# Kernel tuning notes

Measured on AMD Instinct MI355X. Metric: run time of the kernel, lower is better.

Reference implementation:

```python
import jax, jax.numpy as jnp
import numpy as np

B, S, D, H = 2, 2048, 1024, 16
HD = D // H
SCALE = HD ** -0.5


def _xavier(key, fan_out, fan_in):
    limit = (6.0 / (fan_in + fan_out)) ** 0.5
    return jax.random.uniform(key, (fan_out, fan_in), jnp.float32, -limit, limit)


def setup_inputs() -> dict:
    key = jax.random.key(0)
    ks = jax.random.split(key, 11)
    return {
        "q": jax.random.normal(ks[0], (B, S, D), jnp.float32),
        "k": jax.random.normal(ks[1], (B, S, D), jnp.float32),
        "v": jax.random.normal(ks[2], (B, S, D), jnp.float32),
        "Wq": _xavier(ks[3], D, D), "bq": jnp.zeros((D,), jnp.float32),
        "Wk": _xavier(ks[4], D, D), "bk": jnp.zeros((D,), jnp.float32),
        "Wv": _xavier(ks[5], D, D), "bv": jnp.zeros((D,), jnp.float32),
        "Wo": _xavier(ks[6], D, D), "bo": jnp.zeros((D,), jnp.float32),
    }


def reference(q, k, v, Wq, bq, Wk, bk, Wv, bv, Wo, bo):
    # projections: torch Linear is x @ W.T + b
    def split_heads(x):  # [B,S,D] -> [B,H,S,HD]
        return x.reshape(B, S, H, HD).transpose(0, 2, 1, 3)

    qh = split_heads(q @ Wq.T + bq)
    kh = split_heads(k @ Wk.T + bk)
    vh = split_heads(v @ Wv.T + bv)

    scores = jnp.einsum('bhqd,bhkd->bhqk', qh, kh) * SCALE  # [B,H,S,S]
    attn = jax.nn.softmax(scores, axis=-1)
    out = jnp.einsum('bhqk,bhkd->bhqd', attn, vh)  # [B,H,S,HD]
    out = out.transpose(0, 2, 1, 3).reshape(B, S, D)
    return out @ Wo.T + bo
```

## Files before the change

### kernel.cpp

```cpp
#include <hip/hip_runtime.h>
#include <hip/hip_bf16.h>

typedef __attribute__((ext_vector_type(8))) short bf16x8;
typedef __attribute__((ext_vector_type(4))) float f32x4;
typedef __attribute__((ext_vector_type(16))) float f32x16;
typedef unsigned short u16;

#define MFMA16(A,B,C) __builtin_amdgcn_mfma_f32_16x16x32_bf16(A,B,C,0,0,0)
#define MFMA32(A,B,C) __builtin_amdgcn_mfma_f32_32x32x16_bf16(A,B,C,0,0,0)

__device__ __forceinline__ u16 f2bf(float f) {
    union { float f; unsigned u; } x{f};
    unsigned r = x.u + 0x7FFFu + ((x.u >> 16) & 1u);
    return (u16)(r >> 16);
}

__device__ __forceinline__ unsigned cvtpk(float lo, float hi) {
    unsigned r;
    asm("v_cvt_pk_bf16_f32 %0, %1, %2" : "=v"(r) : "v"(lo), "v"(hi));
    return r;
}

__device__ __forceinline__ void gload16(const void* src, void* dst) {
    __builtin_amdgcn_global_load_lds((const __attribute__((address_space(1))) void*)src,
                                     (__attribute__((address_space(3))) void*)dst, 16, 0, 0);
}

__device__ __forceinline__ void xhalf(unsigned lo, unsigned hi2, int hf, unsigned& j0, unsigned& j2) {
#if __has_builtin(__builtin_amdgcn_permlane32_swap)
    auto r = __builtin_amdgcn_permlane32_swap(lo, hi2, false, false);
    j0 = r[0]; j2 = r[1];
#else
    unsigned olo = (unsigned)__shfl_xor((int)lo, 32);
    unsigned ohi = (unsigned)__shfl_xor((int)hi2, 32);
    j0 = hf ? ohi : lo;
    j2 = hf ? hi2 : olo;
#endif
}

__global__ __launch_bounds__(256)
void cvt_in(const float* __restrict__ a, const float* __restrict__ b, const float* __restrict__ c,
            u16* __restrict__ oa, u16* __restrict__ ob, u16* __restrict__ oc) {
    int blk = blockIdx.x; int which = blk >> 11; int lb = blk & 2047;
    const float* s = which == 0 ? a : (which == 1 ? b : c);
    u16* o = which == 0 ? oa : (which == 1 ? ob : oc);
    size_t base = ((size_t)lb * 256 + threadIdx.x) * 8;
    float4 v0 = *(const float4*)(s + base);
    float4 v1 = *(const float4*)(s + base + 4);
    bf16x8 rv;
    rv[0] = (short)f2bf(v0.x); rv[1] = (short)f2bf(v0.y); rv[2] = (short)f2bf(v0.z); rv[3] = (short)f2bf(v0.w);
    rv[4] = (short)f2bf(v1.x); rv[5] = (short)f2bf(v1.y); rv[6] = (short)f2bf(v1.z); rv[7] = (short)f2bf(v1.w);
    *(bf16x8*)(o + base) = rv;
}

__global__ __launch_bounds__(256)
void cvt_w(const float* __restrict__ a, const float* __restrict__ b, const float* __restrict__ c,
           const float* __restrict__ d, u16* __restrict__ o) {
    int blk = blockIdx.x; int which = blk >> 9; int lb = blk & 511;
    const float* s = which == 0 ? a : (which == 1 ? b : (which == 2 ? c : d));
    size_t base = ((size_t)lb * 256 + threadIdx.x) * 8;
    float4 v0 = *(const float4*)(s + base);
    float4 v1 = *(const float4*)(s + base + 4);
    bf16x8 rv;
    rv[0] = (short)f2bf(v0.x); rv[1] = (short)f2bf(v0.y); rv[2] = (short)f2bf(v0.z); rv[3] = (short)f2bf(v0.w);
    rv[4] = (short)f2bf(v1.x); rv[5] = (short)f2bf(v1.y); rv[6] = (short)f2bf(v1.z); rv[7] = (short)f2bf(v1.w);
    *(bf16x8*)(o + (size_t)which * 1048576 + base) = rv;
}

template<int MODE>
__device__ __forceinline__ void gemm_body(u16* gsm, const u16* __restrict__ A, const u16* __restrict__ W,
                                          const float* __restrict__ bias, void* __restrict__ Cout,
                                          float scale) {
    u16* Asl = gsm;
    u16* Wsl = gsm + 16384;
    const int t = threadIdx.x;
    const int lane = t & 63, w = t >> 6;
    const int g = lane >> 4, c = lane & 15;
    const int bm = blockIdx.y * 128, bn = blockIdx.x * 64;
    const int wr = (w >> 1) * 64, wc = (w & 1) * 32;

    f32x4 acc[4][2];
    #pragma unroll
    for (int i = 0; i < 4; ++i) {
        acc[i][0] = f32x4{0.f, 0.f, 0.f, 0.f};
        acc[i][1] = f32x4{0.f, 0.f, 0.f, 0.f};
    }

#define GS(buf, k0)                                                                         \
    {                                                                                       \
        _Pragma("unroll")                                                                   \
        for (int i = 0; i < 4; ++i) {                                                       \
            int off = i * 4096 + w * 1024 + lane * 16;                                      \
            int row = off >> 7, sl = (off >> 4) & 7;                                        \
            gload16(A + (size_t)(bm + row) * 1024 + (k0) + ((sl ^ (row & 7)) << 3),         \
                    Asl + (buf) * 8192 + i * 2048 + w * 512);                               \
        }                                                                                   \
        _Pragma("unroll")                                                                   \
        for (int i = 0; i < 2; ++i) {                                                       \
            int off = i * 4096 + w * 1024 + lane * 16;                                      \
            int row = off >> 7, sl = (off >> 4) & 7;                                        \
            gload16(W + (size_t)(bn + row) * 1024 + (k0) + ((sl ^ (row & 7)) << 3),         \
                    Wsl + (buf) * 4096 + i * 2048 + w * 512);                               \
        }                                                                                   \
    }

    GS(0, 0);
    __syncthreads();
    int cur = 0;

    for (int k0 = 0; k0 < 1024; k0 += 64) {
        if (k0 < 960) GS(cur ^ 1, k0 + 64);
        #pragma unroll
        for (int ks = 0; ks < 2; ++ks) {
            bf16x8 af[4], bfr[2];
            #pragma unroll
            for (int rf = 0; rf < 4; ++rf) {
                int row = wr + rf * 16 + c;
                int col = (ks * 64 + g * 16) ^ ((row & 7) << 4);
                af[rf] = *(const bf16x8*)((const char*)Asl + cur * 16384 + row * 128 + col);
            }
            #pragma unroll
            for (int cf = 0; cf < 2; ++cf) {
                int row = wc + cf * 16 + c;
                int col = (ks * 64 + g * 16) ^ ((row & 7) << 4);
                bfr[cf] = *(const bf16x8*)((const char*)Wsl + cur * 8192 + row * 128 + col);
            }
            #pragma unroll
            for (int rf = 0; rf < 4; ++rf)
                #pragma unroll
                for (int cf = 0; cf < 2; ++cf)
                    acc[rf][cf] = MFMA16(af[rf], bfr[cf], acc[rf][cf]);
        }
        __syncthreads();
        cur ^= 1;
    }
#undef GS

    if (MODE == 2) {
        u16* trp = gsm;
        #pragma unroll
        for (int rf = 0; rf < 4; ++rf)
            #pragma unroll
            for (int cf = 0; cf < 2; ++cf) {
                int d = wc + cf * 16 + c;
                float bv = bias[bn + d];
                unsigned p0 = cvtpk(acc[rf][cf][0] + bv, acc[rf][cf][1] + bv);
                unsigned p1 = cvtpk(acc[rf][cf][2] + bv, acc[rf][cf][3] + bv);
                *(uint2*)&trp[d * 136 + wr + rf * 16 + 4 * g] = make_uint2(p0, p1);
            }
        __syncthreads();
        const int hb = bn >> 6, bb = bm >> 11, sb = bm & 2047;
        u16* vt = (u16*)Cout;
        #pragma unroll
        for (int i = 0; i < 4; ++i) {
            int fl = t + 256 * i;
            int d = fl >> 4, ch = fl & 15;
            bf16x8 vv = *(const bf16x8*)&trp[d * 136 + ch * 8];
            *(bf16x8*)(vt + ((size_t)((bb * 16 + hb) * 64 + d)) * 2048 + sb + ch * 8) = vv;
        }
        return;
    }

    #pragma unroll
    for (int rf = 0; rf < 4; ++rf) {
        #pragma unroll
        for (int cf = 0; cf < 2; ++cf) {
            int nCol = bn + wc + cf * 16 + c;
            float bv = bias[nCol];
            #pragma unroll
            for (int r = 0; r < 4; ++r) {
                int row = bm + wr + rf * 16 + 4 * g + r;
                float val = (acc[rf][cf][r] + bv) * scale;
                if (MODE == 1) ((float*)Cout)[(size_t)row * 1024 + nCol] = val;
                else           ((u16*)Cout)[(size_t)row * 1024 + nCol] = f2bf(val);
            }
        }
    }
}

__global__ __launch_bounds__(256)
void gemm_qkv(const u16* __restrict__ Ab, const u16* __restrict__ Wb,
              const float* __restrict__ b0, const float* __restrict__ b1, const float* __restrict__ b2,
              u16* __restrict__ Qp, u16* __restrict__ Kp, u16* __restrict__ Vtb, float qscale) {
    __shared__ u16 gsm[24576];
    int z = blockIdx.z;
    if (z == 0)      gemm_body<0>(gsm, Ab,           Wb,           b0, Qp,  qscale);
    else if (z == 1) gemm_body<0>(gsm, Ab + 4194304, Wb + 1048576, b1, Kp,  1.f);
    else             gemm_body<2>(gsm, Ab + 8388608, Wb + 2097152, b2, Vtb, 1.f);
}

__global__ __launch_bounds__(256)
void gemm_o(const u16* __restrict__ A, const u16* __restrict__ W,
            const float* __restrict__ bias, float* __restrict__ out) {
    __shared__ u16 gsm[24576];
    gemm_body<1>(gsm, A, W, bias, out, 1.f);
}

__global__ __launch_bounds__(256)
void attn_mfma(const u16* __restrict__ Qp, const u16* __restrict__ Kp,
               const u16* __restrict__ Vt, u16* __restrict__ AO) {
    __shared__ u16 smem[16384];

    const int t = threadIdx.x, lane = t & 63, w = t >> 6;
    const int c5 = lane & 31, hf = lane >> 5;

    const int id = blockIdx.x;
    const int xcd = id & 7, slot = id >> 3;
    const int hd = xcd * 4 + (slot >> 4);
    const int b = hd >> 4, h = hd & 15;
    const int qw = (slot & 15) * 128 + w * 32;

    bf16x8 qfr[4];
    #pragma unroll
    for (int ks = 0; ks < 4; ++ks)
        qfr[ks] = *(const bf16x8*)(Qp + (size_t)(b * 2048 + qw + c5) * 1024 + h * 64 + ks * 16 + hf * 8);

    f32x16 oacc[2], lacc;
    #pragma unroll
    for (int j = 0; j < 16; ++j) { oacc[0][j] = 0.f; oacc[1][j] = 0.f; lacc[j] = 0.f; }

    bf16x8 ones;
    #pragma unroll
    for (int j = 0; j < 8; ++j) ones[j] = (short)0x3F80;

#define STAGE(buf, kt)                                                                              \
    {                                                                                               \
        _Pragma("unroll")                                                                           \
        for (int i = 0; i < 2; ++i) {                                                               \
            int fl = t + 256 * i;                                                                   \
            int row = fl >> 3, sl = fl & 7;                                                         \
            const u16* srck = Kp + (size_t)(b * 2048 + (kt) * 64 + row) * 1024 + h * 64 +           \
                              ((sl ^ (row & 7)) << 3);                                              \
            gload16(srck, smem + (buf) * 4096 + i * 2048 + w * 512);                                \
            const u16* srcv = Vt + ((size_t)((b * 16 + h) * 64 + row)) * 2048 + (kt) * 64 +         \
                              ((sl ^ (row & 7)) << 3);                                              \
            gload16(srcv, smem + 8192 + (buf) * 4096 + i * 2048 + w * 512);                         \
        }                                                                                           \
    }

    STAGE(0, 0);
    __syncthreads();
    int cur = 0;

    for (int kt = 0; kt < 32; ++kt) {
        if (kt < 31) STAGE(cur ^ 1, kt + 1);
        const char* kbase = (const char*)smem + cur * 8192;
        const char* vbase = (const char*)smem + 16384 + cur * 8192;

        #pragma unroll
        for (int kf = 0; kf < 2; ++kf) {
            f32x16 s;
            #pragma unroll
            for (int j = 0; j < 16; ++j) s[j] = 0.f;
            const int krow = kf * 32 + c5;
            const int ksw = (krow & 7) << 4;
            __builtin_amdgcn_s_setprio(1);
            #pragma unroll
            for (int ks = 0; ks < 4; ++ks) {
                bf16x8 ka = *(const bf16x8*)(kbase + krow * 128 + ((ks * 32 + hf * 16) ^ ksw));
                s = MFMA32(ka, qfr[ks], s);
            }
            __builtin_amdgcn_s_setprio(0);

            #pragma unroll
            for (int j = 0; j < 16; ++j) s[j] = exp2f(s[j]);
            unsigned wd[8];
            #pragma unroll
            for (int j = 0; j < 8; ++j) wd[j] = cvtpk(s[2 * j], s[2 * j + 1]);

            union { unsigned u[4]; bf16x8 v; } p0, p1;
            xhalf(wd[0], wd[2], hf, p0.u[0], p0.u[2]);
            xhalf(wd[1], wd[3], hf, p0.u[1], p0.u[3]);
            xhalf(wd[4], wd[6], hf, p1.u[0], p1.u[2]);
            xhalf(wd[5], wd[7], hf, p1.u[1], p1.u[3]);

            __builtin_amdgcn_s_setprio(1);
            #pragma unroll
            for (int pp = 0; pp < 2; ++pp) {
                bf16x8 pB = pp ? p1.v : p0.v;
                const int kc = kf * 64 + pp * 32 + hf * 16;
                #pragma unroll
                for (int df = 0; df < 2; ++df) {
                    int vrow = df * 32 + c5;
                    bf16x8 va = *(const bf16x8*)(vbase + vrow * 128 + (kc ^ ((vrow & 7) << 4)));
                    oacc[df] = MFMA32(va, pB, oacc[df]);
                }
                lacc = MFMA32(ones, pB, lacc);
            }
            __builtin_amdgcn_s_setprio(0);
        }

        __syncthreads();
        cur ^= 1;
    }

    const float inv = 1.f / lacc[0];
    char* pw = (char*)smem + w * 4096;
    #pragma unroll
    for (int df = 0; df < 2; ++df)
        #pragma unroll
        for (int rq = 0; rq < 4; ++rq) {
            unsigned p0 = cvtpk(oacc[df][rq * 4 + 0] * inv, oacc[df][rq * 4 + 1] * inv);
            unsigned p1 = cvtpk(oacc[df][rq * 4 + 2] * inv, oacc[df][rq * 4 + 3] * inv);
            int dbyte = df * 64 + rq * 16 + hf * 8;
            *(uint2*)(pw + c5 * 128 + (dbyte ^ ((c5 & 7) << 4))) = make_uint2(p0, p1);
        }
    #pragma unroll
    for (int i = 0; i < 4; ++i) {
        int fl = lane + 64 * i;
        int q = fl >> 3, ch = fl & 7;
        bf16x8 vv = *(const bf16x8*)(pw + q * 128 + ((ch * 16) ^ ((q & 7) << 4)));
        *(bf16x8*)(AO + (size_t)(b * 2048 + qw + q) * 1024 + h * 64 + ch * 8) = vv;
    }
}

extern "C" void kernel_launch(void* const* d_in, const int* in_sizes, int n_in,
                              void* d_out, int out_size, void* d_ws, size_t ws_size,
                              hipStream_t stream) {
    const float* q  = (const float*)d_in[0];
    const float* k  = (const float*)d_in[1];
    const float* v  = (const float*)d_in[2];
    const float* Wq = (const float*)d_in[3];
    const float* bq = (const float*)d_in[4];
    const float* Wk = (const float*)d_in[5];
    const float* bk = (const float*)d_in[6];
    const float* Wv = (const float*)d_in[7];
    const float* bv = (const float*)d_in[8];
    const float* Wo = (const float*)d_in[9];
    const float* bo = (const float*)d_in[10];

    const size_t NE = 4194304;
    u16* ws = (u16*)d_ws;
    u16* xq = ws;
    u16* xk = ws + NE;
    u16* xv = ws + 2 * NE;
    u16* Wb = ws + 3 * NE;
    u16* Qp = ws + 4 * NE;
    u16* Kp = ws + 5 * NE;
    u16* Vtb = ws + 6 * NE;
    u16* AO = xk;

    const float CS = 0.125f * 1.4426950408889634f;

    cvt_in<<<6144, 256, 0, stream>>>(q, k, v, xq, xk, xv);
    cvt_w<<<2048, 256, 0, stream>>>(Wq, Wk, Wv, Wo, Wb);

    gemm_qkv<<<dim3(16, 32, 3), 256, 0, stream>>>(ws, Wb, bq, bk, bv, Qp, Kp, Vtb, CS);

    attn_mfma<<<512, 256, 0, stream>>>(Qp, Kp, Vtb, AO);

    gemm_o<<<dim3(16, 32), 256, 0, stream>>>(AO, Wb + 3145728, bo, (float*)d_out);
}
```

Measured before the change: 129.4 us.

## Enlarge GEMM tiles to 128x128 and split attention KV range across two wave groups

The projection GEMMs move from 128x64 to 128x128 block tiles with 4x4 MFMA fragments per wave. In exchange they drop double buffering for a single-buffered load-then-sync loop with setprio around the MFMAs. The V-transpose epilogue is rewritten to go through LDS in two passes. The attention kernel now uses 512 threads, where two groups of four waves each process half of the KV tiles, and the partial outputs and row sums are combined through LDS at the end. This aims to raise wave count per block and per-block GEMM reuse, at the cost of exposed load latency and extra reduction and synchronisation.

```diff
diff --git a/kernel.cpp b/kernel.cpp
--- a/kernel.cpp
+++ b/kernel.cpp
@@ -72,91 +72,85 @@
                                           const float* __restrict__ bias, void* __restrict__ Cout,
                                           float scale) {
     u16* Asl = gsm;
-    u16* Wsl = gsm + 16384;
+    u16* Wsl = gsm + 8192;
     const int t = threadIdx.x;
     const int lane = t & 63, w = t >> 6;
     const int g = lane >> 4, c = lane & 15;
-    const int bm = blockIdx.y * 128, bn = blockIdx.x * 64;
-    const int wr = (w >> 1) * 64, wc = (w & 1) * 32;
-
-    f32x4 acc[4][2];
-    #pragma unroll
-    for (int i = 0; i < 4; ++i) {
-        acc[i][0] = f32x4{0.f, 0.f, 0.f, 0.f};
-        acc[i][1] = f32x4{0.f, 0.f, 0.f, 0.f};
-    }
-
-#define GS(buf, k0)                                                                         \
-    {                                                                                       \
-        _Pragma("unroll")                                                                   \
-        for (int i = 0; i < 4; ++i) {                                                       \
-            int off = i * 4096 + w * 1024 + lane * 16;                                      \
-            int row = off >> 7, sl = (off >> 4) & 7;                                        \
-            gload16(A + (size_t)(bm + row) * 1024 + (k0) + ((sl ^ (row & 7)) << 3),         \
-                    Asl + (buf) * 8192 + i * 2048 + w * 512);                               \
-        }                                                                                   \
-        _Pragma("unroll")                                                                   \
-        for (int i = 0; i < 2; ++i) {                                                       \
-            int off = i * 4096 + w * 1024 + lane * 16;                                      \
-            int row = off >> 7, sl = (off >> 4) & 7;                                        \
-            gload16(W + (size_t)(bn + row) * 1024 + (k0) + ((sl ^ (row & 7)) << 3),         \
-                    Wsl + (buf) * 4096 + i * 2048 + w * 512);                               \
-        }                                                                                   \
-    }
-
-    GS(0, 0);
-    __syncthreads();
-    int cur = 0;
+    const int bm = blockIdx.y * 128, bn = blockIdx.x * 128;
+    const int wr = (w >> 1) * 64, wc = (w & 1) * 64;
+
+    f32x4 acc[4][4];
+    #pragma unroll
+    for (int i = 0; i < 4; ++i)
+        #pragma unroll
+        for (int j = 0; j < 4; ++j) acc[i][j] = f32x4{0.f, 0.f, 0.f, 0.f};
 
     for (int k0 = 0; k0 < 1024; k0 += 64) {
-        if (k0 < 960) GS(cur ^ 1, k0 + 64);
+        __syncthreads();
+        #pragma unroll
+        for (int i = 0; i < 4; ++i) {
+            int off = i * 4096 + w * 1024 + lane * 16;
+            int row = off >> 7, sl = (off >> 4) & 7;
+            gload16(A + (size_t)(bm + row) * 1024 + k0 + ((sl ^ (row & 7)) << 3),
+                    Asl + i * 2048 + w * 512);
+            gload16(W + (size_t)(bn + row) * 1024 + k0 + ((sl ^ (row & 7)) << 3),
+                    Wsl + i * 2048 + w * 512);
+        }
+        __syncthreads();
+
         #pragma unroll
         for (int ks = 0; ks < 2; ++ks) {
-            bf16x8 af[4], bfr[2];
+            bf16x8 af[4], bfr[4];
             #pragma unroll
             for (int rf = 0; rf < 4; ++rf) {
                 int row = wr + rf * 16 + c;
                 int col = (ks * 64 + g * 16) ^ ((row & 7) << 4);
-                af[rf] = *(const bf16x8*)((const char*)Asl + cur * 16384 + row * 128 + col);
-            }
-            #pragma unroll
-            for (int cf = 0; cf < 2; ++cf) {
+                af[rf] = *(const bf16x8*)((const char*)Asl + row * 128 + col);
+            }
+            #pragma unroll
+            for (int cf = 0; cf < 4; ++cf) {
                 int row = wc + cf * 16 + c;
                 int col = (ks * 64 + g * 16) ^ ((row & 7) << 4);
-                bfr[cf] = *(const bf16x8*)((const char*)Wsl + cur * 8192 + row * 128 + col);
-            }
+                bfr[cf] = *(const bf16x8*)((const char*)Wsl + row * 128 + col);
+            }
+            __builtin_amdgcn_s_setprio(1);
             #pragma unroll
             for (int rf = 0; rf < 4; ++rf)
                 #pragma unroll
-                for (int cf = 0; cf < 2; ++cf)
+                for (int cf = 0; cf < 4; ++cf)
                     acc[rf][cf] = MFMA16(af[rf], bfr[cf], acc[rf][cf]);
-        }
-        __syncthreads();
-        cur ^= 1;
-    }
-#undef GS
+            __builtin_amdgcn_s_setprio(0);
+        }
+    }
 
     if (MODE == 2) {
-        u16* trp = gsm;
-        #pragma unroll
-        for (int rf = 0; rf < 4; ++rf)
-            #pragma unroll
-            for (int cf = 0; cf < 2; ++cf) {
-                int d = wc + cf * 16 + c;
-                float bv = bias[bn + d];
-                unsigned p0 = cvtpk(acc[rf][cf][0] + bv, acc[rf][cf][1] + bv);
-                unsigned p1 = cvtpk(acc[rf][cf][2] + bv, acc[rf][cf][3] + bv);
-                *(uint2*)&trp[d * 136 + wr + rf * 16 + 4 * g] = make_uint2(p0, p1);
-            }
-        __syncthreads();
-        const int hb = bn >> 6, bb = bm >> 11, sb = bm & 2047;
+        const int bb = bm >> 11, sb = bm & 2047;
         u16* vt = (u16*)Cout;
         #pragma unroll
-        for (int i = 0; i < 4; ++i) {
-            int fl = t + 256 * i;
-            int d = fl >> 4, ch = fl & 15;
-            bf16x8 vv = *(const bf16x8*)&trp[d * 136 + ch * 8];
-            *(bf16x8*)(vt + ((size_t)((bb * 16 + hb) * 64 + d)) * 2048 + sb + ch * 8) = vv;
+        for (int rd = 0; rd < 2; ++rd) {
+            __syncthreads();
+            if ((w & 1) == rd) {
+                #pragma unroll
+                for (int cf = 0; cf < 4; ++cf) {
+                    int dl = cf * 16 + c;
+                    float bv = bias[bn + rd * 64 + dl];
+                    #pragma unroll
+                    for (int rf = 0; rf < 4; ++rf) {
+                        unsigned p0 = cvtpk(acc[rf][cf][0] + bv, acc[rf][cf][1] + bv);
+                        unsigned p1 = cvtpk(acc[rf][cf][2] + bv, acc[rf][cf][3] + bv);
+                        *(uint2*)&gsm[dl * 136 + wr + rf * 16 + 4 * g] = make_uint2(p0, p1);
+                    }
+                }
+            }
+            __syncthreads();
+            const int hrd = (bn >> 6) + rd;
+            #pragma unroll
+            for (int i = 0; i < 4; ++i) {
+                int idx = i * 256 + t;
+                int d = idx >> 4, ch = idx & 15;
+                bf16x8 vv = *(const bf16x8*)&gsm[d * 136 + ch * 8];
+                *(bf16x8*)(vt + ((size_t)((bb * 16 + hrd) * 64 + d)) * 2048 + sb + ch * 8) = vv;
+            }
         }
         return;
     }
@@ -164,7 +158,7 @@
     #pragma unroll
     for (int rf = 0; rf < 4; ++rf) {
         #pragma unroll
-        for (int cf = 0; cf < 2; ++cf) {
+        for (int cf = 0; cf < 4; ++cf) {
             int nCol = bn + wc + cf * 16 + c;
             float bv = bias[nCol];
             #pragma unroll
@@ -182,7 +176,7 @@
 void gemm_qkv(const u16* __restrict__ Ab, const u16* __restrict__ Wb,
               const float* __restrict__ b0, const float* __restrict__ b1, const float* __restrict__ b2,
               u16* __restrict__ Qp, u16* __restrict__ Kp, u16* __restrict__ Vtb, float qscale) {
-    __shared__ u16 gsm[24576];
+    __shared__ u16 gsm[16384];
     int z = blockIdx.z;
     if (z == 0)      gemm_body<0>(gsm, Ab,           Wb,           b0, Qp,  qscale);
     else if (z == 1) gemm_body<0>(gsm, Ab + 4194304, Wb + 1048576, b1, Kp,  1.f);
@@ -192,23 +186,24 @@
 __global__ __launch_bounds__(256)
 void gemm_o(const u16* __restrict__ A, const u16* __restrict__ W,
             const float* __restrict__ bias, float* __restrict__ out) {
-    __shared__ u16 gsm[24576];
+    __shared__ u16 gsm[16384];
     gemm_body<1>(gsm, A, W, bias, out, 1.f);
 }
 
-__global__ __launch_bounds__(256)
+__global__ __launch_bounds__(512, 4)
 void attn_mfma(const u16* __restrict__ Qp, const u16* __restrict__ Kp,
                const u16* __restrict__ Vt, u16* __restrict__ AO) {
-    __shared__ u16 smem[16384];
+    __shared__ u16 smem[32768];
 
     const int t = threadIdx.x, lane = t & 63, w = t >> 6;
+    const int wl = w & 3, half = w >> 2;
     const int c5 = lane & 31, hf = lane >> 5;
 
     const int id = blockIdx.x;
     const int xcd = id & 7, slot = id >> 3;
     const int hd = xcd * 4 + (slot >> 4);
     const int b = hd >> 4, h = hd & 15;
-    const int qw = (slot & 15) * 128 + w * 32;
+    const int qw = (slot & 15) * 128 + wl * 32;
 
     bf16x8 qfr[4];
     #pragma unroll
@@ -223,18 +218,18 @@
     #pragma unroll
     for (int j = 0; j < 8; ++j) ones[j] = (short)0x3F80;
 
-#define STAGE(buf, kt)                                                                              \
+#define STAGE(buf, it)                                                                              \
     {                                                                                               \
+        int row = t >> 3, sl = t & 7;                                                               \
         _Pragma("unroll")                                                                           \
         for (int i = 0; i < 2; ++i) {                                                               \
-            int fl = t + 256 * i;                                                                   \
-            int row = fl >> 3, sl = fl & 7;                                                         \
-            const u16* srck = Kp + (size_t)(b * 2048 + (kt) * 64 + row) * 1024 + h * 64 +           \
+            int kti = i * 16 + (it);                                                                \
+            const u16* srck = Kp + (size_t)(b * 2048 + kti * 64 + row) * 1024 + h * 64 +            \
                               ((sl ^ (row & 7)) << 3);                                              \
-            gload16(srck, smem + (buf) * 4096 + i * 2048 + w * 512);                                \
-            const u16* srcv = Vt + ((size_t)((b * 16 + h) * 64 + row)) * 2048 + (kt) * 64 +         \
+            gload16(srck, smem + i * 8192 + (buf) * 4096 + w * 512);                                \
+            const u16* srcv = Vt + ((size_t)((b * 16 + h) * 64 + row)) * 2048 + kti * 64 +          \
                               ((sl ^ (row & 7)) << 3);                                              \
-            gload16(srcv, smem + 8192 + (buf) * 4096 + i * 2048 + w * 512);                         \
+            gload16(srcv, smem + 16384 + i * 8192 + (buf) * 4096 + w * 512);                        \
         }                                                                                           \
     }
 
@@ -242,10 +237,10 @@
     __syncthreads();
     int cur = 0;
 
-    for (int kt = 0; kt < 32; ++kt) {
-        if (kt < 31) STAGE(cur ^ 1, kt + 1);
-        const char* kbase = (const char*)smem + cur * 8192;
-        const char* vbase = (const char*)smem + 16384 + cur * 8192;
+    for (int it = 0; it < 16; ++it) {
+        if (it < 15) STAGE(cur ^ 1, it + 1);
+        const char* kbase = (const char*)smem + half * 16384 + cur * 8192;
+        const char* vbase = (const char*)smem + 32768 + half * 16384 + cur * 8192;
 
         #pragma unroll
         for (int kf = 0; kf < 2; ++kf) {
@@ -294,23 +289,42 @@
         cur ^= 1;
     }
 
-    const float inv = 1.f / lacc[0];
-    char* pw = (char*)smem + w * 4096;
-    #pragma unroll
-    for (int df = 0; df < 2; ++df)
-        #pragma unroll
-        for (int rq = 0; rq < 4; ++rq) {
-            unsigned p0 = cvtpk(oacc[df][rq * 4 + 0] * inv, oacc[df][rq * 4 + 1] * inv);
-            unsigned p1 = cvtpk(oacc[df][rq * 4 + 2] * inv, oacc[df][rq * 4 + 3] * inv);
-            int dbyte = df * 64 + rq * 16 + hf * 8;
-            *(uint2*)(pw + c5 * 128 + (dbyte ^ ((c5 & 7) << 4))) = make_uint2(p0, p1);
-        }
-    #pragma unroll
-    for (int i = 0; i < 4; ++i) {
-        int fl = lane + 64 * i;
-        int q = fl >> 3, ch = fl & 7;
-        bf16x8 vv = *(const bf16x8*)(pw + q * 128 + ((ch * 16) ^ ((q & 7) << 4)));
-        *(bf16x8*)(AO + (size_t)(b * 2048 + qw + q) * 1024 + h * 64 + ch * 8) = vv;
+    float* fs = (float*)smem;
+    const int pbase = wl * 2112;
+    if (half) {
+        #pragma unroll
+        for (int df = 0; df < 2; ++df)
+            #pragma unroll
+            for (int j = 0; j < 16; ++j)
+                fs[pbase + (df * 16 + j) * 64 + lane] = oacc[df][j];
+        fs[pbase + 2048 + lane] = lacc[0];
+    }
+    __syncthreads();
+    if (!half) {
+        #pragma unroll
+        for (int df = 0; df < 2; ++df)
+            #pragma unroll
+            for (int j = 0; j < 16; ++j)
+                oacc[df][j] += fs[pbase + (df * 16 + j) * 64 + lane];
+        const float inv = 1.f / (lacc[0] + fs[pbase + 2048 + lane]);
+
+        char* pw = (char*)smem + 33792 + wl * 4096;
+        #pragma unroll
+        for (int df = 0; df < 2; ++df)
+            #pragma unroll
+            for (int rq = 0; rq < 4; ++rq) {
+                unsigned p0 = cvtpk(oacc[df][rq * 4 + 0] * inv, oacc[df][rq * 4 + 1] * inv);
+                unsigned p1 = cvtpk(oacc[df][rq * 4 + 2] * inv, oacc[df][rq * 4 + 3] * inv);
+                int dbyte = df * 64 + rq * 16 + hf * 8;
+                *(uint2*)(pw + c5 * 128 + (dbyte ^ ((c5 & 7) << 4))) = make_uint2(p0, p1);
+            }
+        #pragma unroll
+        for (int i = 0; i < 4; ++i) {
+            int fl = lane + 64 * i;
+            int q = fl >> 3, ch = fl & 7;
+            bf16x8 vv = *(const bf16x8*)(pw + q * 128 + ((ch * 16) ^ ((q & 7) << 4)));
+            *(bf16x8*)(AO + (size_t)(b * 2048 + qw + q) * 1024 + h * 64 + ch * 8) = vv;
+        }
     }
 }
 
@@ -345,9 +359,9 @@
     cvt_in<<<6144, 256, 0, stream>>>(q, k, v, xq, xk, xv);
     cvt_w<<<2048, 256, 0, stream>>>(Wq, Wk, Wv, Wo, Wb);
 
-    gemm_qkv<<<dim3(16, 32, 3), 256, 0, stream>>>(ws, Wb, bq, bk, bv, Qp, Kp, Vtb, CS);
-
-    attn_mfma<<<512, 256, 0, stream>>>(Qp, Kp, Vtb, AO);
-
-    gemm_o<<<dim3(16, 32), 256, 0, stream>>>(AO, Wb + 3145728, bo, (float*)d_out);
-}
+    gemm_qkv<<<dim3(8, 32, 3), 256, 0, stream>>>(ws, Wb, bq, bk, bv, Qp, Kp, Vtb, CS);
+
+    attn_mfma<<<512, 512, 0, stream>>>(Qp, Kp, Vtb, AO);
+
+    gemm_o<<<dim3(8, 32), 256, 0, stream>>>(AO, Wb + 3145728, bo, (float*)d_out);
+}
```

Measured after the change: 139.5 us. 1.08x slower.

## Split attention KV loop across two wave groups, merge convert kernels, prioritize GEMM MFMA

Applied to the files above, without the earlier changes.

The attention kernel now launches 512 threads per block, and two groups of four waves each process half of the key/value tiles for the same query rows. The partial outputs and row sums are combined through shared memory before normalization. Shared memory per block doubles to stage both halves. The two fp32-to-bf16 conversion kernels are merged into one launch, and the GEMM MFMA block is wrapped in s_setprio hints. The aim is more waves in flight to hide latency during attention, plus one fewer launch, at the cost of an extra reduction step and more LDS use.

```diff
diff --git a/kernel.cpp b/kernel.cpp
--- a/kernel.cpp
+++ b/kernel.cpp
@@ -39,32 +39,31 @@
 }
 
 __global__ __launch_bounds__(256)
-void cvt_in(const float* __restrict__ a, const float* __restrict__ b, const float* __restrict__ c,
-            u16* __restrict__ oa, u16* __restrict__ ob, u16* __restrict__ oc) {
-    int blk = blockIdx.x; int which = blk >> 11; int lb = blk & 2047;
-    const float* s = which == 0 ? a : (which == 1 ? b : c);
-    u16* o = which == 0 ? oa : (which == 1 ? ob : oc);
-    size_t base = ((size_t)lb * 256 + threadIdx.x) * 8;
+void cvt_all(const float* __restrict__ q, const float* __restrict__ k, const float* __restrict__ v,
+             const float* __restrict__ Wq, const float* __restrict__ Wk,
+             const float* __restrict__ Wv, const float* __restrict__ Wo,
+             u16* __restrict__ oq, u16* __restrict__ ok, u16* __restrict__ ov,
+             u16* __restrict__ ow) {
+    int blk = blockIdx.x;
+    const float* s;
+    u16* o;
+    if (blk < 6144) {
+        int which = blk >> 11, lb = blk & 2047;
+        s = (which == 0 ? q : (which == 1 ? k : v)) + (size_t)lb * 2048;
+        o = (which == 0 ? oq : (which == 1 ? ok : ov)) + (size_t)lb * 2048;
+    } else {
+        int wblk = blk - 6144;
+        int which = wblk >> 9, lb = wblk & 511;
+        s = (which == 0 ? Wq : (which == 1 ? Wk : (which == 2 ? Wv : Wo))) + (size_t)lb * 2048;
+        o = ow + (size_t)which * 1048576 + (size_t)lb * 2048;
+    }
+    size_t base = (size_t)threadIdx.x * 8;
     float4 v0 = *(const float4*)(s + base);
     float4 v1 = *(const float4*)(s + base + 4);
     bf16x8 rv;
     rv[0] = (short)f2bf(v0.x); rv[1] = (short)f2bf(v0.y); rv[2] = (short)f2bf(v0.z); rv[3] = (short)f2bf(v0.w);
     rv[4] = (short)f2bf(v1.x); rv[5] = (short)f2bf(v1.y); rv[6] = (short)f2bf(v1.z); rv[7] = (short)f2bf(v1.w);
     *(bf16x8*)(o + base) = rv;
-}
-
-__global__ __launch_bounds__(256)
-void cvt_w(const float* __restrict__ a, const float* __restrict__ b, const float* __restrict__ c,
-           const float* __restrict__ d, u16* __restrict__ o) {
-    int blk = blockIdx.x; int which = blk >> 9; int lb = blk & 511;
-    const float* s = which == 0 ? a : (which == 1 ? b : (which == 2 ? c : d));
-    size_t base = ((size_t)lb * 256 + threadIdx.x) * 8;
-    float4 v0 = *(const float4*)(s + base);
-    float4 v1 = *(const float4*)(s + base + 4);
-    bf16x8 rv;
-    rv[0] = (short)f2bf(v0.x); rv[1] = (short)f2bf(v0.y); rv[2] = (short)f2bf(v0.z); rv[3] = (short)f2bf(v0.w);
-    rv[4] = (short)f2bf(v1.x); rv[5] = (short)f2bf(v1.y); rv[6] = (short)f2bf(v1.z); rv[7] = (short)f2bf(v1.w);
-    *(bf16x8*)(o + (size_t)which * 1048576 + base) = rv;
 }
 
 template<int MODE>
@@ -125,11 +124,13 @@
                 int col = (ks * 64 + g * 16) ^ ((row & 7) << 4);
                 bfr[cf] = *(const bf16x8*)((const char*)Wsl + cur * 8192 + row * 128 + col);
             }
+            __builtin_amdgcn_s_setprio(1);
             #pragma unroll
             for (int rf = 0; rf < 4; ++rf)
                 #pragma unroll
                 for (int cf = 0; cf < 2; ++cf)
                     acc[rf][cf] = MFMA16(af[rf], bfr[cf], acc[rf][cf]);
+            __builtin_amdgcn_s_setprio(0);
         }
         __syncthreads();
         cur ^= 1;
@@ -196,19 +197,20 @@
     gemm_body<1>(gsm, A, W, bias, out, 1.f);
 }
 
-__global__ __launch_bounds__(256)
+__global__ __launch_bounds__(512, 4)
 void attn_mfma(const u16* __restrict__ Qp, const u16* __restrict__ Kp,
                const u16* __restrict__ Vt, u16* __restrict__ AO) {
-    __shared__ u16 smem[16384];
+    __shared__ u16 smem[32768];
 
     const int t = threadIdx.x, lane = t & 63, w = t >> 6;
+    const int wl = w & 3, half = w >> 2;
     const int c5 = lane & 31, hf = lane >> 5;
 
     const int id = blockIdx.x;
     const int xcd = id & 7, slot = id >> 3;
     const int hd = xcd * 4 + (slot >> 4);
     const int b = hd >> 4, h = hd & 15;
-    const int qw = (slot & 15) * 128 + w * 32;
+    const int qw = (slot & 15) * 128 + wl * 32;
 
     bf16x8 qfr[4];
     #pragma unroll
@@ -223,18 +225,18 @@
     #pragma unroll
     for (int j = 0; j < 8; ++j) ones[j] = (short)0x3F80;
 
-#define STAGE(buf, kt)                                                                              \
+#define STAGE(buf, it)                                                                              \
     {                                                                                               \
+        int row = t >> 3, sl = t & 7;                                                               \
         _Pragma("unroll")                                                                           \
         for (int i = 0; i < 2; ++i) {                                                               \
-            int fl = t + 256 * i;                                                                   \
-            int row = fl >> 3, sl = fl & 7;                                                         \
-            const u16* srck = Kp + (size_t)(b * 2048 + (kt) * 64 + row) * 1024 + h * 64 +           \
+            int kti = i * 16 + (it);                                                                \
+            const u16* srck = Kp + (size_t)(b * 2048 + kti * 64 + row) * 1024 + h * 64 +            \
                               ((sl ^ (row & 7)) << 3);                                              \
-            gload16(srck, smem + (buf) * 4096 + i * 2048 + w * 512);                                \
-            const u16* srcv = Vt + ((size_t)((b * 16 + h) * 64 + row)) * 2048 + (kt) * 64 +         \
+            gload16(srck, smem + i * 8192 + (buf) * 4096 + w * 512);                                \
+            const u16* srcv = Vt + ((size_t)((b * 16 + h) * 64 + row)) * 2048 + kti * 64 +          \
                               ((sl ^ (row & 7)) << 3);                                              \
-            gload16(srcv, smem + 8192 + (buf) * 4096 + i * 2048 + w * 512);                         \
+            gload16(srcv, smem + 16384 + i * 8192 + (buf) * 4096 + w * 512);                        \
         }                                                                                           \
     }
 
@@ -242,10 +244,10 @@
     __syncthreads();
     int cur = 0;
 
-    for (int kt = 0; kt < 32; ++kt) {
-        if (kt < 31) STAGE(cur ^ 1, kt + 1);
-        const char* kbase = (const char*)smem + cur * 8192;
-        const char* vbase = (const char*)smem + 16384 + cur * 8192;
+    for (int it = 0; it < 16; ++it) {
+        if (it < 15) STAGE(cur ^ 1, it + 1);
+        const char* kbase = (const char*)smem + half * 16384 + cur * 8192;
+        const char* vbase = (const char*)smem + 32768 + half * 16384 + cur * 8192;
 
         #pragma unroll
         for (int kf = 0; kf < 2; ++kf) {
@@ -294,23 +296,42 @@
         cur ^= 1;
     }
 
-    const float inv = 1.f / lacc[0];
-    char* pw = (char*)smem + w * 4096;
-    #pragma unroll
-    for (int df = 0; df < 2; ++df)
-        #pragma unroll
-        for (int rq = 0; rq < 4; ++rq) {
-            unsigned p0 = cvtpk(oacc[df][rq * 4 + 0] * inv, oacc[df][rq * 4 + 1] * inv);
-            unsigned p1 = cvtpk(oacc[df][rq * 4 + 2] * inv, oacc[df][rq * 4 + 3] * inv);
-            int dbyte = df * 64 + rq * 16 + hf * 8;
-            *(uint2*)(pw + c5 * 128 + (dbyte ^ ((c5 & 7) << 4))) = make_uint2(p0, p1);
-        }
-    #pragma unroll
-    for (int i = 0; i < 4; ++i) {
-        int fl = lane + 64 * i;
-        int q = fl >> 3, ch = fl & 7;
-        bf16x8 vv = *(const bf16x8*)(pw + q * 128 + ((ch * 16) ^ ((q & 7) << 4)));
-        *(bf16x8*)(AO + (size_t)(b * 2048 + qw + q) * 1024 + h * 64 + ch * 8) = vv;
+    float* fs = (float*)smem;
+    const int pbase = wl * 2112;
+    if (half) {
+        #pragma unroll
+        for (int df = 0; df < 2; ++df)
+            #pragma unroll
+            for (int j = 0; j < 16; ++j)
+                fs[pbase + (df * 16 + j) * 64 + lane] = oacc[df][j];
+        fs[pbase + 2048 + lane] = lacc[0];
+    }
+    __syncthreads();
+    if (!half) {
+        #pragma unroll
+        for (int df = 0; df < 2; ++df)
+            #pragma unroll
+            for (int j = 0; j < 16; ++j)
+                oacc[df][j] += fs[pbase + (df * 16 + j) * 64 + lane];
+        const float inv = 1.f / (lacc[0] + fs[pbase + 2048 + lane]);
+
+        char* pw = (char*)smem + 33792 + wl * 4096;
+        #pragma unroll
+        for (int df = 0; df < 2; ++df)
+            #pragma unroll
+            for (int rq = 0; rq < 4; ++rq) {
+                unsigned p0 = cvtpk(oacc[df][rq * 4 + 0] * inv, oacc[df][rq * 4 + 1] * inv);
+                unsigned p1 = cvtpk(oacc[df][rq * 4 + 2] * inv, oacc[df][rq * 4 + 3] * inv);
+                int dbyte = df * 64 + rq * 16 + hf * 8;
+                *(uint2*)(pw + c5 * 128 + (dbyte ^ ((c5 & 7) << 4))) = make_uint2(p0, p1);
+            }
+        #pragma unroll
+        for (int i = 0; i < 4; ++i) {
+            int fl = lane + 64 * i;
+            int q = fl >> 3, ch = fl & 7;
+            bf16x8 vv = *(const bf16x8*)(pw + q * 128 + ((ch * 16) ^ ((q & 7) << 4)));
+            *(bf16x8*)(AO + (size_t)(b * 2048 + qw + q) * 1024 + h * 64 + ch * 8) = vv;
+        }
     }
 }
 
@@ -342,12 +363,11 @@
 
     const float CS = 0.125f * 1.4426950408889634f;
 
-    cvt_in<<<6144, 256, 0, stream>>>(q, k, v, xq, xk, xv);
-    cvt_w<<<2048, 256, 0, stream>>>(Wq, Wk, Wv, Wo, Wb);
+    cvt_all<<<8192, 256, 0, stream>>>(q, k, v, Wq, Wk, Wv, Wo, xq, xk, xv, Wb);
 
     gemm_qkv<<<dim3(16, 32, 3), 256, 0, stream>>>(ws, Wb, bq, bk, bv, Qp, Kp, Vtb, CS);
 
-    attn_mfma<<<512, 256, 0, stream>>>(Qp, Kp, Vtb, AO);
+    attn_mfma<<<512, 512, 0, stream>>>(Qp, Kp, Vtb, AO);
 
     gemm_o<<<dim3(16, 32), 256, 0, stream>>>(AO, Wb + 3145728, bo, (float*)d_out);
 }
```

New measurement: 121.6 us. -6.0%, faster.
